# Kernel optimization log

Measured on AMD Instinct MI355X. Metric: run time of the kernel, lower is better.

Reference implementation:

```python
import jax, jax.numpy as jnp
import numpy as np

B, T, C, H = 4, 2048, 1024, 16
HD = C // H
INIT_SCALE = 0.25

def setup_inputs() -> dict:
    key = jax.random.key(0)
    k1, k2, k3 = jax.random.split(key, 3)
    x = jax.random.normal(k1, (B, T, C), dtype=jnp.float32)
    W_attn = jax.random.normal(k2, (3 * C, C), dtype=jnp.float32) * INIT_SCALE  # torch Linear weight [out,in]
    b_attn = jnp.zeros((3 * C,), dtype=jnp.float32)
    W_proj = jax.random.normal(k3, (C, C), dtype=jnp.float32) * INIT_SCALE
    b_proj = jnp.zeros((C,), dtype=jnp.float32)
    return {"x": x, "W_attn": W_attn, "b_attn": b_attn, "W_proj": W_proj, "b_proj": b_proj}

def reference(x, W_attn, b_attn, W_proj, b_proj):
    # fused QKV projection: [B,T,3C]
    qkv = x @ W_attn.T + b_attn
    q, k, v = jnp.split(qkv, 3, axis=-1)  # each [B,T,C]
    # [B,H,T,HD]
    q = q.reshape(B, T, H, HD).transpose(0, 2, 1, 3)
    k = k.reshape(B, T, H, HD).transpose(0, 2, 1, 3)
    v = v.reshape(B, T, H, HD).transpose(0, 2, 1, 3)
    scale = 1.0 / jnp.sqrt(jnp.asarray(HD, dtype=q.dtype))
    attn = jnp.einsum('bhqd,bhkd->bhqk', q, k) * scale  # [B,H,T,T]
    attn = jax.nn.softmax(attn, axis=-1)
    out = jnp.einsum('bhqk,bhkd->bhqd', attn, v)  # [B,H,T,HD]
    out = out.transpose(0, 2, 1, 3).reshape(B, T, C)
    return out @ W_proj.T + b_proj
```

## Files before the change

### kernel.cpp

```cpp
#include <hip/hip_runtime.h>
#include <hip/hip_bf16.h>

#define BB 4
#define TT 2048
#define CC 1024
#define HH 16
#define HD 64

typedef _Float16 half8 __attribute__((ext_vector_type(8)));
typedef _Float16 half4 __attribute__((ext_vector_type(4)));
typedef _Float16 half2_t __attribute__((ext_vector_type(2)));
typedef float floatx4 __attribute__((ext_vector_type(4)));

__device__ __forceinline__ void async_cp16(const void* g, void* l) {
    __builtin_amdgcn_global_load_lds(
        (const __attribute__((address_space(1))) unsigned int*)g,
        (__attribute__((address_space(3))) unsigned int*)l,
        16, 0, 0);
}

__global__ void cvt_f32_f16(const float* __restrict__ src, _Float16* __restrict__ dst, int n) {
    int i = (blockIdx.x * blockDim.x + threadIdx.x) * 8;
    if (i < n) {
        float4 v0 = *(const float4*)(src + i);
        float4 v1 = *(const float4*)(src + i + 4);
        half8 h;
        h[0] = (_Float16)v0.x; h[1] = (_Float16)v0.y; h[2] = (_Float16)v0.z; h[3] = (_Float16)v0.w;
        h[4] = (_Float16)v1.x; h[5] = (_Float16)v1.y; h[6] = (_Float16)v1.z; h[7] = (_Float16)v1.w;
        *(half8*)(dst + i) = h;
    }
}

template <int EPI>
__global__ __launch_bounds__(256) void hgemm_nt(
    const _Float16* __restrict__ A, const _Float16* __restrict__ Bw,
    const float* __restrict__ bias,
    _Float16* __restrict__ q_out, _Float16* __restrict__ k_out, _Float16* __restrict__ v_out,
    float* __restrict__ c_out,
    int M, int N, int K)
{
    __shared__ __attribute__((aligned(16))) _Float16 As[128 * 32];
    __shared__ __attribute__((aligned(16))) _Float16 Bs[128 * 32];

    const int tid  = threadIdx.x;
    const int lane = tid & 63;
    const int wave = tid >> 6;
    const int quad = lane >> 4;
    const int lc   = lane & 15;
    const int wr   = wave >> 1, wc = wave & 1;
    const size_t bm = (size_t)blockIdx.y * 128;
    const size_t bn = (size_t)blockIdx.x * 128;

    const int r0 = tid >> 2;
    const int ck = (tid & 3) * 8;

    const _Float16* Ap0 = A + (bm + r0) * (size_t)K + ck;
    const _Float16* Ap1 = A + (bm + 64 + r0) * (size_t)K + ck;
    const _Float16* Bp0 = Bw + (bn + r0) * (size_t)K + ck;
    const _Float16* Bp1 = Bw + (bn + 64 + r0) * (size_t)K + ck;
    _Float16* lA0 = As + tid * 8;
    _Float16* lA1 = As + 2048 + tid * 8;
    _Float16* lB0 = Bs + tid * 8;
    _Float16* lB1 = Bs + 2048 + tid * 8;

    floatx4 acc[4][4] = {};

    for (int kk = 0; kk < K; kk += 32) {
        __syncthreads();
        async_cp16(Ap0 + kk, lA0);
        async_cp16(Ap1 + kk, lA1);
        async_cp16(Bp0 + kk, lB0);
        async_cp16(Bp1 + kk, lB1);
        __syncthreads();

        half8 af[4], bf[4];
#pragma unroll
        for (int mt = 0; mt < 4; mt++) af[mt] = *(const half8*)(As + (wr * 64 + mt * 16 + lc) * 32 + quad * 8);
#pragma unroll
        for (int nt = 0; nt < 4; nt++) bf[nt] = *(const half8*)(Bs + (wc * 64 + nt * 16 + lc) * 32 + quad * 8);
#pragma unroll
        for (int mt = 0; mt < 4; mt++)
#pragma unroll
            for (int nt = 0; nt < 4; nt++)
                acc[mt][nt] = __builtin_amdgcn_mfma_f32_16x16x32_f16(af[mt], bf[nt], acc[mt][nt], 0, 0, 0);
    }

#pragma unroll
    for (int mt = 0; mt < 4; mt++) {
        int mbase = (int)bm + wr * 64 + mt * 16 + quad * 4;
#pragma unroll
        for (int nt = 0; nt < 4; nt++) {
            int n = (int)bn + wc * 64 + nt * 16 + lc;
            float bv = bias[n];
#pragma unroll
            for (int r = 0; r < 4; r++) {
                float v = acc[mt][nt][r] + bv;
                int mm = mbase + r;
                if (EPI == 0) {
                    int seg = n >> 10;
                    int cm  = n & 1023;
                    int h = cm >> 6, d = cm & 63;
                    int bb = mm >> 11, t = mm & 2047;
                    size_t dst = (((size_t)(bb * HH + h)) * TT + t) * HD + d;
                    if (seg == 0)      q_out[dst] = (_Float16)(v * 0.18033688f);
                    else if (seg == 1) k_out[dst] = (_Float16)v;
                    else               v_out[dst] = (_Float16)v;
                } else {
                    c_out[(size_t)mm * N + n] = v;
                }
            }
        }
    }
}

__global__ __launch_bounds__(512) void attn_flash(
    const _Float16* __restrict__ Qp, const _Float16* __restrict__ Kp,
    const _Float16* __restrict__ Vp, _Float16* __restrict__ Op)
{
    __shared__ __attribute__((aligned(16))) _Float16 Ks[64][72];
    __shared__ __attribute__((aligned(16))) _Float16 Vt[64][76];

    const int bh   = blockIdx.x;
    const int qt   = blockIdx.y;
    const int tid  = threadIdx.x;
    const int lane = tid & 63;
    const int wave = tid >> 6;
    const int quad = lane >> 4;
    const int lc   = lane & 15;

    const size_t hb = (size_t)bh * TT * HD;
    const _Float16* Kh = Kp + hb;
    const _Float16* Vh = Vp + hb;

    const int q0row = qt * 256 + wave * 32 + lc;
    const int q1row = q0row + 16;
    half8 bq00 = *(const half8*)(Qp + hb + (size_t)q0row * HD + quad * 8);
    half8 bq01 = *(const half8*)(Qp + hb + (size_t)q0row * HD + 32 + quad * 8);
    half8 bq10 = *(const half8*)(Qp + hb + (size_t)q1row * HD + quad * 8);
    half8 bq11 = *(const half8*)(Qp + hb + (size_t)q1row * HD + 32 + quad * 8);

    floatx4 o0[4] = {}, o1[4] = {};
    float m0 = -1e30f, l0 = 0.f, m1 = -1e30f, l1 = 0.f;

    const int sk  = tid >> 3;
    const int sc0 = (tid & 7) * 8;
    const int vkp = tid >> 4;
    const int vd4 = (tid & 15) * 4;

    const _Float16* Kg  = Kh + (size_t)sk * HD + sc0;
    const _Float16* Vg0 = Vh + (size_t)(2 * vkp) * HD + vd4;
    const _Float16* Vg1 = Vg0 + HD;

    for (int kt = 0; kt < TT; kt += 64) {
        const size_t koff = (size_t)kt * HD;
        half8 kv  = *(const half8*)(Kg + koff);
        half4 va0 = *(const half4*)(Vg0 + koff);
        half4 vb0 = *(const half4*)(Vg1 + koff);
        __syncthreads();
        *(half8*)&Ks[sk][sc0] = kv;
#pragma unroll
        for (int j = 0; j < 4; j++) {
            half2_t w; w[0] = va0[j]; w[1] = vb0[j];
            *(half2_t*)&Vt[vd4 + j][2 * vkp] = w;
        }
        __syncthreads();

        floatx4 s0[4], s1[4];
        const floatx4 zf = {0.f, 0.f, 0.f, 0.f};
#pragma unroll
        for (int m = 0; m < 4; m++) {
            half8 a0 = *(const half8*)&Ks[m * 16 + lc][quad * 8];
            half8 a1 = *(const half8*)&Ks[m * 16 + lc][32 + quad * 8];
            s0[m] = __builtin_amdgcn_mfma_f32_16x16x32_f16(a0, bq00, zf, 0, 0, 0);
            s0[m] = __builtin_amdgcn_mfma_f32_16x16x32_f16(a1, bq01, s0[m], 0, 0, 0);
            s1[m] = __builtin_amdgcn_mfma_f32_16x16x32_f16(a0, bq10, zf, 0, 0, 0);
            s1[m] = __builtin_amdgcn_mfma_f32_16x16x32_f16(a1, bq11, s1[m], 0, 0, 0);
        }

        half4 pf0[4], pf1[4];
        {
            float mx = s0[0][0];
#pragma unroll
            for (int m = 0; m < 4; m++)
#pragma unroll
                for (int r = 0; r < 4; r++) mx = fmaxf(mx, s0[m][r]);
            mx = fmaxf(mx, __shfl_xor(mx, 16));
            mx = fmaxf(mx, __shfl_xor(mx, 32));
            float mnew = fmaxf(m0, mx);
            float al = exp2f(m0 - mnew);
            m0 = mnew;
            float rs = 0.f;
#pragma unroll
            for (int m = 0; m < 4; m++) {
                float p0 = exp2f(s0[m][0] - mnew);
                float p1 = exp2f(s0[m][1] - mnew);
                float p2 = exp2f(s0[m][2] - mnew);
                float p3 = exp2f(s0[m][3] - mnew);
                rs += (p0 + p1) + (p2 + p3);
                half4 t;
                t[0] = (_Float16)p0; t[1] = (_Float16)p1;
                t[2] = (_Float16)p2; t[3] = (_Float16)p3;
                pf0[m] = t;
            }
            rs += __shfl_xor(rs, 16);
            rs += __shfl_xor(rs, 32);
            l0 = l0 * al + rs;
#pragma unroll
            for (int dt = 0; dt < 4; dt++) o0[dt] *= al;
        }
        {
            float mx = s1[0][0];
#pragma unroll
            for (int m = 0; m < 4; m++)
#pragma unroll
                for (int r = 0; r < 4; r++) mx = fmaxf(mx, s1[m][r]);
            mx = fmaxf(mx, __shfl_xor(mx, 16));
            mx = fmaxf(mx, __shfl_xor(mx, 32));
            float mnew = fmaxf(m1, mx);
            float al = exp2f(m1 - mnew);
            m1 = mnew;
            float rs = 0.f;
#pragma unroll
            for (int m = 0; m < 4; m++) {
                float p0 = exp2f(s1[m][0] - mnew);
                float p1 = exp2f(s1[m][1] - mnew);
                float p2 = exp2f(s1[m][2] - mnew);
                float p3 = exp2f(s1[m][3] - mnew);
                rs += (p0 + p1) + (p2 + p3);
                half4 t;
                t[0] = (_Float16)p0; t[1] = (_Float16)p1;
                t[2] = (_Float16)p2; t[3] = (_Float16)p3;
                pf1[m] = t;
            }
            rs += __shfl_xor(rs, 16);
            rs += __shfl_xor(rs, 32);
            l1 = l1 * al + rs;
#pragma unroll
            for (int dt = 0; dt < 4; dt++) o1[dt] *= al;
        }

#pragma unroll
        for (int dt = 0; dt < 4; dt++) {
            const _Float16* vr = &Vt[dt * 16 + lc][quad * 4];
#pragma unroll
            for (int m = 0; m < 4; m++) {
                half4 va = *(const half4*)(vr + m * 16);
                o0[dt] = __builtin_amdgcn_mfma_f32_16x16x16f16(va, pf0[m], o0[dt], 0, 0, 0);
                o1[dt] = __builtin_amdgcn_mfma_f32_16x16x16f16(va, pf1[m], o1[dt], 0, 0, 0);
            }
        }
    }

    const int b = bh >> 4, h = bh & 15;
    {
        float inv = 1.0f / l0;
        size_t base = ((size_t)(b * TT + q0row)) * CC + h * HD;
#pragma unroll
        for (int dt = 0; dt < 4; dt++) {
            half4 hv;
#pragma unroll
            for (int r = 0; r < 4; r++) hv[r] = (_Float16)(o0[dt][r] * inv);
            *(half4*)(Op + base + dt * 16 + quad * 4) = hv;
        }
    }
    {
        float inv = 1.0f / l1;
        size_t base = ((size_t)(b * TT + q1row)) * CC + h * HD;
#pragma unroll
        for (int dt = 0; dt < 4; dt++) {
            half4 hv;
#pragma unroll
            for (int r = 0; r < 4; r++) hv[r] = (_Float16)(o1[dt][r] * inv);
            *(half4*)(Op + base + dt * 16 + quad * 4) = hv;
        }
    }
}

extern "C" void kernel_launch(void* const* d_in, const int* in_sizes, int n_in,
                              void* d_out, int out_size, void* d_ws, size_t ws_size,
                              hipStream_t stream) {
    const float* x      = (const float*)d_in[0];
    const float* W_attn = (const float*)d_in[1];
    const float* b_attn = (const float*)d_in[2];
    const float* W_proj = (const float*)d_in[3];
    const float* b_proj = (const float*)d_in[4];
    float* out = (float*)d_out;

    const size_t SZ_XH  = (size_t)BB * TT * CC * 2;
    const size_t SZ_WA  = (size_t)3 * CC * CC * 2;
    const size_t SZ_WP  = (size_t)CC * CC * 2;
    const size_t SZ_QKV = (size_t)BB * HH * TT * HD * 2;
    size_t off = 0;
    _Float16* xh  = (_Float16*)((char*)d_ws + off); off += SZ_XH;
    _Float16* wah = (_Float16*)((char*)d_ws + off); off += SZ_WA;
    _Float16* wph = (_Float16*)((char*)d_ws + off); off += SZ_WP;
    _Float16* Qh  = (_Float16*)((char*)d_ws + off); off += SZ_QKV;
    _Float16* Kh  = (_Float16*)((char*)d_ws + off); off += SZ_QKV;
    _Float16* Vh  = (_Float16*)((char*)d_ws + off); off += SZ_QKV;
    _Float16* Ah  = (_Float16*)((char*)d_ws + off); off += SZ_XH;
    if (ws_size < off) return;

    const int NX  = BB * TT * CC;
    const int NWA = 3 * CC * CC;
    const int NWP = CC * CC;
    cvt_f32_f16<<<NX / 8 / 256, 256, 0, stream>>>(x, xh, NX);
    cvt_f32_f16<<<NWA / 8 / 256, 256, 0, stream>>>(W_attn, wah, NWA);
    cvt_f32_f16<<<NWP / 8 / 256, 256, 0, stream>>>(W_proj, wph, NWP);

    hgemm_nt<0><<<dim3(3 * CC / 128, BB * TT / 128), 256, 0, stream>>>(
        xh, wah, b_attn, Qh, Kh, Vh, nullptr, BB * TT, 3 * CC, CC);

    attn_flash<<<dim3(BB * HH, TT / 256), 512, 0, stream>>>(Qh, Kh, Vh, Ah);

    hgemm_nt<1><<<dim3(CC / 128, BB * TT / 128), 256, 0, stream>>>(
        Ah, wph, b_proj, nullptr, nullptr, nullptr, out, BB * TT, CC, CC);
}
```

Measured before the change: 326.5 us.

## Merge conversion kernels, stage QKV epilogue through LDS, shrink attention blocks

Three fp32-to-fp16 conversion launches become one kernel that picks its source by index range, which removes two launches. The QKV GEMM epilogue now writes its tile into shared memory first and then stores each head row as contiguous 16-byte vectors, replacing scattered 2-byte stores. The attention kernel goes from 512 to 256 threads per block over 128 query rows, doubling the grid and giving each thread wider K/V tile loads. The cost is a larger LDS allocation for the QKV GEMM and fewer waves per block sharing each K/V tile, so K/V is loaded from global memory twice as often.

```diff
diff --git a/kernel.cpp b/kernel.cpp
--- a/kernel.cpp
+++ b/kernel.cpp
@@ -6,6 +6,9 @@
 #define CC 1024
 #define HH 16
 #define HD 64
+#define NX  (BB * TT * CC)
+#define NWA (3 * CC * CC)
+#define NWP (CC * CC)
 
 typedef _Float16 half8 __attribute__((ext_vector_type(8)));
 typedef _Float16 half4 __attribute__((ext_vector_type(4)));
@@ -19,16 +22,21 @@
         16, 0, 0);
 }
 
-__global__ void cvt_f32_f16(const float* __restrict__ src, _Float16* __restrict__ dst, int n) {
+__global__ void cvt_all(const float* __restrict__ x, const float* __restrict__ wa,
+                        const float* __restrict__ wp,
+                        _Float16* __restrict__ xh, _Float16* __restrict__ wah,
+                        _Float16* __restrict__ wph) {
     int i = (blockIdx.x * blockDim.x + threadIdx.x) * 8;
-    if (i < n) {
-        float4 v0 = *(const float4*)(src + i);
-        float4 v1 = *(const float4*)(src + i + 4);
-        half8 h;
-        h[0] = (_Float16)v0.x; h[1] = (_Float16)v0.y; h[2] = (_Float16)v0.z; h[3] = (_Float16)v0.w;
-        h[4] = (_Float16)v1.x; h[5] = (_Float16)v1.y; h[6] = (_Float16)v1.z; h[7] = (_Float16)v1.w;
-        *(half8*)(dst + i) = h;
-    }
+    const float* s; _Float16* d; int j;
+    if (i < NX)            { s = x;  d = xh;  j = i; }
+    else if (i < NX + NWA) { s = wa; d = wah; j = i - NX; }
+    else                   { s = wp; d = wph; j = i - NX - NWA; }
+    float4 v0 = *(const float4*)(s + j);
+    float4 v1 = *(const float4*)(s + j + 4);
+    half8 h;
+    h[0] = (_Float16)v0.x; h[1] = (_Float16)v0.y; h[2] = (_Float16)v0.z; h[3] = (_Float16)v0.w;
+    h[4] = (_Float16)v1.x; h[5] = (_Float16)v1.y; h[6] = (_Float16)v1.z; h[7] = (_Float16)v1.w;
+    *(half8*)(d + j) = h;
 }
 
 template <int EPI>
@@ -39,8 +47,9 @@
     float* __restrict__ c_out,
     int M, int N, int K)
 {
-    __shared__ __attribute__((aligned(16))) _Float16 As[128 * 32];
-    __shared__ __attribute__((aligned(16))) _Float16 Bs[128 * 32];
+    __shared__ __attribute__((aligned(16))) _Float16 Sm[EPI == 0 ? 128 * 132 : 8192];
+    _Float16* As = Sm;
+    _Float16* Bs = Sm + 4096;
 
     const int tid  = threadIdx.x;
     const int lane = tid & 63;
@@ -85,35 +94,59 @@
                 acc[mt][nt] = __builtin_amdgcn_mfma_f32_16x16x32_f16(af[mt], bf[nt], acc[mt][nt], 0, 0, 0);
     }
 
-#pragma unroll
-    for (int mt = 0; mt < 4; mt++) {
-        int mbase = (int)bm + wr * 64 + mt * 16 + quad * 4;
-#pragma unroll
-        for (int nt = 0; nt < 4; nt++) {
-            int n = (int)bn + wc * 64 + nt * 16 + lc;
-            float bv = bias[n];
-#pragma unroll
-            for (int r = 0; r < 4; r++) {
-                float v = acc[mt][nt][r] + bv;
-                int mm = mbase + r;
-                if (EPI == 0) {
-                    int seg = n >> 10;
-                    int cm  = n & 1023;
-                    int h = cm >> 6, d = cm & 63;
-                    int bb = mm >> 11, t = mm & 2047;
-                    size_t dst = (((size_t)(bb * HH + h)) * TT + t) * HD + d;
-                    if (seg == 0)      q_out[dst] = (_Float16)(v * 0.18033688f);
-                    else if (seg == 1) k_out[dst] = (_Float16)v;
-                    else               v_out[dst] = (_Float16)v;
-                } else {
-                    c_out[(size_t)mm * N + n] = v;
+    if (EPI == 0) {
+        const int seg = (int)(bn >> 10);
+        __syncthreads();
+#pragma unroll
+        for (int mt = 0; mt < 4; mt++) {
+            int m_loc = wr * 64 + mt * 16 + quad * 4;
+#pragma unroll
+            for (int nt = 0; nt < 4; nt++) {
+                int n_loc = wc * 64 + nt * 16 + lc;
+                float bv = bias[bn + n_loc];
+#pragma unroll
+                for (int r = 0; r < 4; r++) {
+                    float v = acc[mt][nt][r] + bv;
+                    if (seg == 0) v *= 0.18033688f;
+                    Sm[(m_loc + r) * 132 + n_loc] = (_Float16)v;
                 }
             }
         }
-    }
-}
-
-__global__ __launch_bounds__(512) void attn_flash(
+        __syncthreads();
+        const int m_loc = tid >> 1, nh = tid & 1;
+        const int mm = (int)bm + m_loc;
+        const int nbase = (int)bn + nh * 64;
+        const int h = (nbase & 1023) >> 6;
+        const int bb = mm >> 11, t = mm & 2047;
+        size_t db = (((size_t)(bb * HH + h)) * TT + t) * HD;
+        _Float16* dst = (seg == 0) ? (q_out + db) : (seg == 1) ? (k_out + db) : (v_out + db);
+        const _Float16* src = Sm + m_loc * 132 + nh * 64;
+#pragma unroll
+        for (int j = 0; j < 8; j++) {
+            half4 lo = *(const half4*)(src + j * 8);
+            half4 hi = *(const half4*)(src + j * 8 + 4);
+            half8 w;
+            w[0] = lo[0]; w[1] = lo[1]; w[2] = lo[2]; w[3] = lo[3];
+            w[4] = hi[0]; w[5] = hi[1]; w[6] = hi[2]; w[7] = hi[3];
+            *(half8*)(dst + j * 8) = w;
+        }
+    } else {
+#pragma unroll
+        for (int mt = 0; mt < 4; mt++) {
+            int mbase = (int)bm + wr * 64 + mt * 16 + quad * 4;
+#pragma unroll
+            for (int nt = 0; nt < 4; nt++) {
+                int n = (int)bn + wc * 64 + nt * 16 + lc;
+                float bv = bias[n];
+#pragma unroll
+                for (int r = 0; r < 4; r++)
+                    c_out[(size_t)(mbase + r) * N + n] = acc[mt][nt][r] + bv;
+            }
+        }
+    }
+}
+
+__global__ __launch_bounds__(256) void attn_flash(
     const _Float16* __restrict__ Qp, const _Float16* __restrict__ Kp,
     const _Float16* __restrict__ Vp, _Float16* __restrict__ Op)
 {
@@ -132,7 +165,7 @@
     const _Float16* Kh = Kp + hb;
     const _Float16* Vh = Vp + hb;
 
-    const int q0row = qt * 256 + wave * 32 + lc;
+    const int q0row = qt * 128 + wave * 32 + lc;
     const int q1row = q0row + 16;
     half8 bq00 = *(const half8*)(Qp + hb + (size_t)q0row * HD + quad * 8);
     half8 bq01 = *(const half8*)(Qp + hb + (size_t)q0row * HD + 32 + quad * 8);
@@ -142,26 +175,28 @@
     floatx4 o0[4] = {}, o1[4] = {};
     float m0 = -1e30f, l0 = 0.f, m1 = -1e30f, l1 = 0.f;
 
-    const int sk  = tid >> 3;
-    const int sc0 = (tid & 7) * 8;
-    const int vkp = tid >> 4;
-    const int vd4 = (tid & 15) * 4;
+    const int sk  = tid >> 2;
+    const int sc0 = (tid & 3) * 16;
+    const int vkp = tid >> 3;
+    const int vd8 = (tid & 7) * 8;
 
     const _Float16* Kg  = Kh + (size_t)sk * HD + sc0;
-    const _Float16* Vg0 = Vh + (size_t)(2 * vkp) * HD + vd4;
+    const _Float16* Vg0 = Vh + (size_t)(2 * vkp) * HD + vd8;
     const _Float16* Vg1 = Vg0 + HD;
 
     for (int kt = 0; kt < TT; kt += 64) {
         const size_t koff = (size_t)kt * HD;
-        half8 kv  = *(const half8*)(Kg + koff);
-        half4 va0 = *(const half4*)(Vg0 + koff);
-        half4 vb0 = *(const half4*)(Vg1 + koff);
-        __syncthreads();
-        *(half8*)&Ks[sk][sc0] = kv;
-#pragma unroll
-        for (int j = 0; j < 4; j++) {
-            half2_t w; w[0] = va0[j]; w[1] = vb0[j];
-            *(half2_t*)&Vt[vd4 + j][2 * vkp] = w;
+        half8 kv0 = *(const half8*)(Kg + koff);
+        half8 kv1 = *(const half8*)(Kg + koff + 8);
+        half8 va  = *(const half8*)(Vg0 + koff);
+        half8 vb  = *(const half8*)(Vg1 + koff);
+        __syncthreads();
+        *(half8*)&Ks[sk][sc0]     = kv0;
+        *(half8*)&Ks[sk][sc0 + 8] = kv1;
+#pragma unroll
+        for (int j = 0; j < 8; j++) {
+            half2_t w; w[0] = va[j]; w[1] = vb[j];
+            *(half2_t*)&Vt[vd8 + j][2 * vkp] = w;
         }
         __syncthreads();
 
@@ -244,9 +279,9 @@
             const _Float16* vr = &Vt[dt * 16 + lc][quad * 4];
 #pragma unroll
             for (int m = 0; m < 4; m++) {
-                half4 va = *(const half4*)(vr + m * 16);
-                o0[dt] = __builtin_amdgcn_mfma_f32_16x16x16f16(va, pf0[m], o0[dt], 0, 0, 0);
-                o1[dt] = __builtin_amdgcn_mfma_f32_16x16x16f16(va, pf1[m], o1[dt], 0, 0, 0);
+                half4 vfr = *(const half4*)(vr + m * 16);
+                o0[dt] = __builtin_amdgcn_mfma_f32_16x16x16f16(vfr, pf0[m], o0[dt], 0, 0, 0);
+                o1[dt] = __builtin_amdgcn_mfma_f32_16x16x16f16(vfr, pf1[m], o1[dt], 0, 0, 0);
             }
         }
     }
@@ -286,9 +321,9 @@
     const float* b_proj = (const float*)d_in[4];
     float* out = (float*)d_out;
 
-    const size_t SZ_XH  = (size_t)BB * TT * CC * 2;
-    const size_t SZ_WA  = (size_t)3 * CC * CC * 2;
-    const size_t SZ_WP  = (size_t)CC * CC * 2;
+    const size_t SZ_XH  = (size_t)NX * 2;
+    const size_t SZ_WA  = (size_t)NWA * 2;
+    const size_t SZ_WP  = (size_t)NWP * 2;
     const size_t SZ_QKV = (size_t)BB * HH * TT * HD * 2;
     size_t off = 0;
     _Float16* xh  = (_Float16*)((char*)d_ws + off); off += SZ_XH;
@@ -300,17 +335,13 @@
     _Float16* Ah  = (_Float16*)((char*)d_ws + off); off += SZ_XH;
     if (ws_size < off) return;
 
-    const int NX  = BB * TT * CC;
-    const int NWA = 3 * CC * CC;
-    const int NWP = CC * CC;
-    cvt_f32_f16<<<NX / 8 / 256, 256, 0, stream>>>(x, xh, NX);
-    cvt_f32_f16<<<NWA / 8 / 256, 256, 0, stream>>>(W_attn, wah, NWA);
-    cvt_f32_f16<<<NWP / 8 / 256, 256, 0, stream>>>(W_proj, wph, NWP);
+    cvt_all<<<(NX + NWA + NWP) / 8 / 256, 256, 0, stream>>>(
+        x, W_attn, W_proj, xh, wah, wph);
 
     hgemm_nt<0><<<dim3(3 * CC / 128, BB * TT / 128), 256, 0, stream>>>(
         xh, wah, b_attn, Qh, Kh, Vh, nullptr, BB * TT, 3 * CC, CC);
 
-    attn_flash<<<dim3(BB * HH, TT / 256), 512, 0, stream>>>(Qh, Kh, Vh, Ah);
+    attn_flash<<<dim3(BB * HH, TT / 128), 256, 0, stream>>>(Qh, Kh, Vh, Ah);
 
     hgemm_nt<1><<<dim3(CC / 128, BB * TT / 128), 256, 0, stream>>>(
         Ah, wph, b_proj, nullptr, nullptr, nullptr, out, BB * TT, CC, CC);
```

New measurement: 355.0 us. 1.09x slower.
